# Optimization experiments

Measured on AMD Instinct MI355X. Metric: run time of the kernel, lower is better.

The kernel has to match this reference:

```python
import jax, jax.numpy as jnp
import numpy as np

B, S, HID = 2, 1024, 1024
NH, CH, HD = 16, 32, 64          # standard heads, constitutional heads, head_dim
TRUST = 64


def setup_inputs() -> dict:
    key = jax.random.key(0)
    ks = jax.random.split(key, 16)
    g = lambda k, sh, sc: jax.random.normal(k, sh, dtype=jnp.float32) * sc
    w = 1.0 / np.sqrt(HID)
    inp = {
        'hidden_states': g(ks[0], (B, S, HID), 1.0),
        'attention_mask': g(ks[1], (B, 1, S, S), 1.0),
        'trust_scores': jax.random.uniform(ks[2], (B, TRUST), dtype=jnp.float32),
        'Wq': g(ks[3], (HID, HID), w), 'bq': jnp.zeros((HID,), jnp.float32),
        'Wk': g(ks[4], (HID, HID), w), 'bk': jnp.zeros((HID,), jnp.float32),
        'Wv': g(ks[5], (HID, HID), w), 'bv': jnp.zeros((HID,), jnp.float32),
        'Wcq': g(ks[6], (HID, CH * HD), w), 'bcq': jnp.zeros((CH * HD,), jnp.float32),
        'Wck': g(ks[7], (HID, CH * HD), w), 'bck': jnp.zeros((CH * HD,), jnp.float32),
        'Wcv': g(ks[8], (HID, CH * HD), w), 'bcv': jnp.zeros((CH * HD,), jnp.float32),
        'Wt': g(ks[9], (TRUST, NH), 1.0 / np.sqrt(TRUST)), 'bt': jnp.zeros((NH,), jnp.float32),
        'Wo': g(ks[10], (HID, HID), w), 'bo': jnp.zeros((HID,), jnp.float32),
    }
    return inp


def reference(hidden_states, attention_mask, trust_scores,
              Wq, bq, Wk, bk, Wv, bv,
              Wcq, bcq, Wck, bck, Wcv, bcv,
              Wt, bt, Wo, bo):
    x = hidden_states
    scale = 1.0 / np.sqrt(HD).astype(np.float32)

    # standard QKV -> [B, NH, S, HD]
    q = (x @ Wq + bq).reshape(B, S, NH, HD)
    k = (x @ Wk + bk).reshape(B, S, NH, HD)
    v = (x @ Wv + bv).reshape(B, S, NH, HD)
    scores = jnp.einsum('bqhd,bkhd->bhqk', q, k) * scale  # [B,NH,S,S]
    scores = scores + attention_mask                       # additive mask

    # constitutional QKV -> [B, CH, S, HD]
    cq = (x @ Wcq + bcq).reshape(B, S, CH, HD)
    ck = (x @ Wck + bck).reshape(B, S, CH, HD)
    const_scores = jnp.einsum('bqhd,bkhd->bhqk', cq, ck) * scale  # [B,CH,S,S]

    # trust weighting: [B,TRUST] -> [B,NH] broadcast over [S,S]
    tw = trust_scores @ Wt + bt
    scores = scores * tw[:, :, None, None]

    # combine: per-head scores + mean over constitutional heads
    combined = scores + jnp.mean(const_scores, axis=1, keepdims=True)
    probs = jax.nn.softmax(combined, axis=-1)  # dropout is identity in eval

    context = jnp.einsum('bhqk,bkhd->bqhd', probs, v).reshape(B, S, HID)
    output = context @ Wo + bo
    return output, probs


if __name__ == '__main__':
    out, probs = reference(**setup_inputs())
    print(out.shape, probs.shape)
```

## Files before the change

kernel.cpp:

```cpp
#include <hip/hip_runtime.h>


typedef __bf16 bf16x8 __attribute__((ext_vector_type(8)));
typedef __bf16 bf16x4 __attribute__((ext_vector_type(4)));
typedef float  f32x4  __attribute__((ext_vector_type(4)));

static constexpr int Sq  = 1024;
static constexpr int LDP = 7168;

template<int ROWS>
__device__ __forceinline__ void stage_g(const __bf16* g, int ld, __bf16* s, int tid)
{
    constexpr int PER = (ROWS * 4) / 256;
    int w = tid >> 6, l = tid & 63;
#pragma unroll
    for (int i = 0; i < PER; i++) {
        int bc = w * 64 + i * 256;
        int chunk = bc + l;
        int row = chunk >> 2, part = (chunk & 3) * 8;
        const __bf16* gp = g + (size_t)row * ld + part;
        __bf16* sp = s + (size_t)bc * 8;
        __builtin_amdgcn_global_load_lds(
            (__attribute__((address_space(1))) void*)(gp),
            (__attribute__((address_space(3))) void*)(sp), 16, 0, 0);
    }
}

template<int BM, int BN, int EPI>
__global__ __launch_bounds__(256) void gemm_nt(
    const __bf16* __restrict__ A, int lda,
    const __bf16* __restrict__ B, int ldb,
    void* __restrict__ Cout, int ldc,
    const float* __restrict__ bias, int Ksz, float alpha)
{
    constexpr int WM = BM / 2, WN = BN / 2, FM = WM / 16, FN = WN / 16;
    __shared__ __bf16 As[BM][32];
    __shared__ __bf16 Bs[BN][32];
    int tid = threadIdx.x;
    int w = tid >> 6, l = tid & 63;
    int wr = w >> 1, wc = w & 1;
    int lr = l & 15, kp = (l >> 4) * 8;
    int bm = blockIdx.x * BM, bn = blockIdx.y * BN;
    int z = blockIdx.z;

    size_t zA = 0, zC = 0;
    if constexpr (EPI == 2) { zA = (size_t)z * 1024 * LDP; zC = (size_t)z * Sq * Sq; }

    f32x4 acc[FM][FN];
#pragma unroll
    for (int i = 0; i < FM; i++)
#pragma unroll
        for (int j = 0; j < FN; j++) acc[i][j] = (f32x4){0.f, 0.f, 0.f, 0.f};

    for (int k0 = 0; k0 < Ksz; k0 += 32) {
        stage_g<BM>(A + zA + (size_t)bm * lda + k0, lda, &As[0][0], tid);
        stage_g<BN>(B + zA + (size_t)bn * ldb + k0, ldb, &Bs[0][0], tid);
        __syncthreads();
        bf16x8 av[FM], bv[FN];
#pragma unroll
        for (int i = 0; i < FM; i++) av[i] = *(const bf16x8*)&As[wr * WM + i * 16 + lr][kp];
#pragma unroll
        for (int j = 0; j < FN; j++) bv[j] = *(const bf16x8*)&Bs[wc * WN + j * 16 + lr][kp];
#pragma unroll
        for (int i = 0; i < FM; i++)
#pragma unroll
            for (int j = 0; j < FN; j++)
                acc[i][j] = __builtin_amdgcn_mfma_f32_16x16x32_bf16(av[i], bv[j], acc[i][j], 0, 0, 0);
        __syncthreads();
    }

    int dr = (l >> 4) * 4, dc = l & 15;
#pragma unroll
    for (int i = 0; i < FM; i++)
#pragma unroll
        for (int j = 0; j < FN; j++)
#pragma unroll
            for (int t = 0; t < 4; t++) {
                int row = bm + wr * WM + i * 16 + dr + t;
                int col = bn + wc * WN + j * 16 + dc;
                float v = acc[i][j][t];
                size_t off = zC + (size_t)row * ldc + col;
                if constexpr (EPI == 0)      ((__bf16*)Cout)[off] = (__bf16)(v + bias[col]);
                else if constexpr (EPI == 1) ((float*)Cout)[off]  = v + bias[col];
                else                         ((float*)Cout)[off]  = v * alpha;
            }
}

__global__ __launch_bounds__(256, 2) void attn_fused(
    const __bf16* __restrict__ PROJ, const __bf16* __restrict__ Vt,
    const float* __restrict__ mask, const float* __restrict__ CM,
    const float* __restrict__ TW, float* __restrict__ probs,
    __bf16* __restrict__ CTXb)
{
    __shared__ float ctxred[4][64][36];
    __shared__ float red[32][4];

    int tid = threadIdx.x;
    int w = tid >> 6, l = tid & 63;
    int lr = l & 15, g = l >> 4, kp = g * 8;

    int bid = blockIdx.x;
    int low3 = bid & 7;
    int t6   = bid >> 3;
    int h    = t6 & 15;
    int g64  = (t6 >> 4) * 8 + low3;
    int b    = g64 >> 5;
    int bm   = (g64 & 31) * 32;
    int z    = b * 16 + h;

    const __bf16* Qg = PROJ + (size_t)(b * 1024 + bm) * LDP + h * 64;
    const __bf16* Kg = PROJ + (size_t)(b * 1024) * LDP + 1024 + h * 64;

    bf16x8 qv[2][2];
#pragma unroll
    for (int i = 0; i < 2; i++)
#pragma unroll
        for (int kk = 0; kk < 2; kk++)
            qv[i][kk] = *(const bf16x8*)(Qg + (size_t)(i * 16 + lr) * LDP + kk * 32 + kp);

    f32x4 acc[2][16];
#pragma unroll
    for (int i = 0; i < 2; i++)
#pragma unroll
        for (int j = 0; j < 16; j++) acc[i][j] = (f32x4){0.f, 0.f, 0.f, 0.f};

#pragma unroll
    for (int j = 0; j < 16; j++) {
        const __bf16* Kt = Kg + (size_t)(w * 256 + j * 16 + lr) * LDP;
        bf16x8 k0 = *(const bf16x8*)(Kt + kp);
        bf16x8 k1 = *(const bf16x8*)(Kt + 32 + kp);
#pragma unroll
        for (int i = 0; i < 2; i++) {
            acc[i][j] = __builtin_amdgcn_mfma_f32_16x16x32_bf16(k0, qv[i][0], acc[i][j], 0, 0, 0);
            acc[i][j] = __builtin_amdgcn_mfma_f32_16x16x32_bf16(k1, qv[i][1], acc[i][j], 0, 0, 0);
        }
    }

    float twv = TW[z];
    float s1 = 0.125f * twv;
    const float* Mb  = mask + (size_t)b * Sq * Sq;
    const float* CMb = CM   + (size_t)b * Sq * Sq;

    float mx[2];
#pragma unroll
    for (int i = 0; i < 2; i++) {
        size_t rb = (size_t)(bm + i * 16 + lr) * 1024;
        float mm = -1e30f;
#pragma unroll
        for (int j = 0; j < 16; j++) {
            int off = w * 256 + j * 16 + g * 4;
            f32x4 mk = *(const f32x4*)(Mb + rb + off);
            f32x4 c4 = *(const f32x4*)(CMb + rb + off);
#pragma unroll
            for (int t = 0; t < 4; t++) {
                float lv = fmaf(acc[i][j][t], s1, fmaf(mk[t], twv, c4[t]));
                acc[i][j][t] = lv;
                mm = fmaxf(mm, lv);
            }
        }
        mm = fmaxf(mm, __shfl_xor(mm, 16));
        mm = fmaxf(mm, __shfl_xor(mm, 32));
        mx[i] = mm;
    }
    if (g == 0) { red[lr][w] = mx[0]; red[16 + lr][w] = mx[1]; }
    __syncthreads();
#pragma unroll
    for (int i = 0; i < 2; i++) {
        const float* r = red[i * 16 + lr];
        mx[i] = fmaxf(fmaxf(r[0], r[1]), fmaxf(r[2], r[3]));
    }

    float sm[2];
#pragma unroll
    for (int i = 0; i < 2; i++) {
        float s = 0.f;
#pragma unroll
        for (int j = 0; j < 16; j++)
#pragma unroll
            for (int t = 0; t < 4; t++) {
                float e = __expf(acc[i][j][t] - mx[i]);
                acc[i][j][t] = e;
                s += e;
            }
        s += __shfl_xor(s, 16);
        s += __shfl_xor(s, 32);
        sm[i] = s;
    }
    __syncthreads();
    if (g == 0) { red[lr][w] = sm[0]; red[16 + lr][w] = sm[1]; }
    __syncthreads();

    float inv[2];
#pragma unroll
    for (int i = 0; i < 2; i++) {
        const float* r = red[i * 16 + lr];
        inv[i] = 1.0f / (r[0] + r[1] + r[2] + r[3]);
    }

    const __bf16* Vg = Vt + ((size_t)b * 1024 + h * 64) * 1024;
    float* Pg = probs + (size_t)z * Sq * Sq;
    f32x4 c[2][4];
#pragma unroll
    for (int i = 0; i < 2; i++)
#pragma unroll
        for (int nt = 0; nt < 4; nt++) c[i][nt] = (f32x4){0.f, 0.f, 0.f, 0.f};

#pragma unroll
    for (int j = 0; j < 16; j++) {
        int kb = w * 256 + j * 16 + g * 4;
        bf16x4 vb[4];
#pragma unroll
        for (int nt = 0; nt < 4; nt++)
            vb[nt] = *(const bf16x4*)(Vg + (size_t)(nt * 16 + lr) * 1024 + kb);
#pragma unroll
        for (int i = 0; i < 2; i++) {
            f32x4 p;
#pragma unroll
            for (int t = 0; t < 4; t++) p[t] = acc[i][j][t] * inv[i];
            *(f32x4*)(Pg + (size_t)(bm + i * 16 + lr) * 1024 + kb) = p;
            bf16x4 pa;
#pragma unroll
            for (int t = 0; t < 4; t++) pa[t] = (__bf16)p[t];
#pragma unroll
            for (int nt = 0; nt < 4; nt++)
                asm volatile("v_mfma_f32_16x16x16_bf16 %0, %1, %2, %0"
                             : "+v"(c[i][nt]) : "v"(pa), "v"(vb[nt]));
        }
    }

#pragma unroll
    for (int i = 0; i < 2; i++)
#pragma unroll
        for (int nt = 0; nt < 4; nt++)
            *(f32x4*)&ctxred[w][nt * 16 + lr][i * 16 + g * 4] = c[i][nt];
    __syncthreads();

    int q8 = tid & 31, dq = (tid >> 5) * 8;
    bf16x8 o;
#pragma unroll
    for (int e = 0; e < 8; e++) {
        int d = dq + e;
        float s = ctxred[0][d][q8] + ctxred[1][d][q8] + ctxred[2][d][q8] + ctxred[3][d][q8];
        o[e] = (__bf16)s;
    }
    *(bf16x8*)&CTXb[(size_t)(b * 1024 + bm + q8) * 1024 + h * 64 + dq] = o;
}

__global__ __launch_bounds__(256) void convert_f32_bf16(
    const float* __restrict__ src, __bf16* __restrict__ dst)
{
    int i = blockIdx.x * 256 + threadIdx.x;
    size_t base = (size_t)i * 8;
    float4 a = *(const float4*)(src + base);
    float4 b = *(const float4*)(src + base + 4);
    bf16x8 o;
    o[0] = (__bf16)a.x; o[1] = (__bf16)a.y; o[2] = (__bf16)a.z; o[3] = (__bf16)a.w;
    o[4] = (__bf16)b.x; o[5] = (__bf16)b.y; o[6] = (__bf16)b.z; o[7] = (__bf16)b.w;
    *(bf16x8*)(dst + base) = o;
}

__global__ __launch_bounds__(256) void transpose_all(
    const float* __restrict__ Wq, const float* __restrict__ Wk,
    const float* __restrict__ Wv, const float* __restrict__ Wcq,
    const float* __restrict__ Wck, const float* __restrict__ Wo,
    __bf16* __restrict__ Wall, __bf16* __restrict__ WoT)
{
    int zz = blockIdx.z;
    const float* src;
    int nof, ld;
    switch (zz) {
        case 0: src = Wq;  nof = 0;    ld = 1024; break;
        case 1: src = Wk;  nof = 0;    ld = 1024; break;
        case 2: src = Wv;  nof = 0;    ld = 1024; break;
        case 3: src = Wcq; nof = 0;    ld = 2048; break;
        case 4: src = Wcq; nof = 1024; ld = 2048; break;
        case 5: src = Wck; nof = 0;    ld = 2048; break;
        case 6: src = Wck; nof = 1024; ld = 2048; break;
        default: src = Wo; nof = 0;    ld = 1024; break;
    }
    __bf16* dst = (zz == 7) ? WoT : Wall + (size_t)zz * 1024 * 1024;

    __shared__ float t[32][33];
    int tx = threadIdx.x, ty = threadIdx.y;
    int n0 = blockIdx.x * 32, k0 = blockIdx.y * 32;
#pragma unroll
    for (int i = 0; i < 4; i++)
        t[ty + i * 8][tx] = src[(size_t)(k0 + ty + i * 8) * ld + nof + n0 + tx];
    __syncthreads();
#pragma unroll
    for (int i = 0; i < 4; i++)
        dst[(size_t)(n0 + ty + i * 8) * 1024 + k0 + tx] = (__bf16)t[tx][ty + i * 8];
}

__global__ __launch_bounds__(256) void transpose_v(
    const __bf16* __restrict__ PROJ, __bf16* __restrict__ Vt)
{
    int b = blockIdx.z;
    __shared__ __bf16 t[32][33];
    int tx = threadIdx.x, ty = threadIdx.y;
    int s0 = blockIdx.x * 32, d0 = blockIdx.y * 32;
#pragma unroll
    for (int i = 0; i < 4; i++)
        t[ty + i * 8][tx] = PROJ[(size_t)(b * 1024 + s0 + ty + i * 8) * LDP + 2048 + d0 + tx];
    __syncthreads();
#pragma unroll
    for (int i = 0; i < 4; i++)
        Vt[(size_t)(b * 1024 + d0 + ty + i * 8) * 1024 + s0 + tx] = t[tx][ty + i * 8];
}

__global__ void pack_bias(const float* bq, const float* bk, const float* bv,
                          const float* bcq, const float* bck, float* ball)
{
    int i = blockIdx.x * 256 + threadIdx.x;
    if (i >= LDP) return;
    float v;
    if (i < 1024) v = bq[i];
    else if (i < 2048) v = bk[i - 1024];
    else if (i < 3072) v = bv[i - 2048];
    else if (i < 5120) v = bcq[i - 3072];
    else v = bck[i - 5120];
    ball[i] = v;
}

__global__ void tw_kernel(const float* __restrict__ trust, const float* __restrict__ Wt,
                          const float* __restrict__ bt, float* __restrict__ tw)
{
    int i = threadIdx.x;
    if (i >= 32) return;
    int b = i >> 4, h = i & 15;
    float s = bt[h];
    for (int k = 0; k < 64; k++) s += trust[b * 64 + k] * Wt[k * 16 + h];
    tw[i] = s;
}

extern "C" void kernel_launch(void* const* d_in, const int* in_sizes, int n_in,
                              void* d_out, int out_size, void* d_ws, size_t ws_size,
                              hipStream_t stream)
{
    (void)in_sizes; (void)n_in; (void)out_size; (void)ws_size;
    const float* x     = (const float*)d_in[0];
    const float* mask  = (const float*)d_in[1];
    const float* trust = (const float*)d_in[2];
    const float* Wq  = (const float*)d_in[3];  const float* bq  = (const float*)d_in[4];
    const float* Wk  = (const float*)d_in[5];  const float* bk  = (const float*)d_in[6];
    const float* Wv  = (const float*)d_in[7];  const float* bv  = (const float*)d_in[8];
    const float* Wcq = (const float*)d_in[9];  const float* bcq = (const float*)d_in[10];
    const float* Wck = (const float*)d_in[11]; const float* bck = (const float*)d_in[12];
    const float* Wt  = (const float*)d_in[15]; const float* bt  = (const float*)d_in[16];
    const float* Wo  = (const float*)d_in[17]; const float* bo  = (const float*)d_in[18];

    float* out   = (float*)d_out;
    float* probs = out + (size_t)2 * Sq * 1024;

    constexpr size_t MB = 1u << 20;
    char* w8 = (char*)d_ws;
    __bf16* xb   = (__bf16*)(w8 + 0 * MB);
    __bf16* Wall = (__bf16*)(w8 + 4 * MB);
    float*  ball = (float*) (w8 + 19 * MB);
    float*  TW   = (float*) (w8 + 19 * MB + 65536);
    __bf16* WoT  = (__bf16*)(w8 + 19 * MB + 131072);
    __bf16* PROJ = (__bf16*)(w8 + 22 * MB);
    __bf16* Vt   = (__bf16*)(w8 + 50 * MB);
    float*  CM   = (float*) (w8 + 54 * MB);
    __bf16* CTXb = (__bf16*)(w8 + 0 * MB);

    dim3 tb(32, 8);

    convert_f32_bf16<<<1024, 256, 0, stream>>>(x, xb);
    transpose_all<<<dim3(32, 32, 8), tb, 0, stream>>>(Wq, Wk, Wv, Wcq, Wck, Wo, Wall, WoT);
    pack_bias<<<28, 256, 0, stream>>>(bq, bk, bv, bcq, bck, ball);
    tw_kernel<<<1, 64, 0, stream>>>(trust, Wt, bt, TW);

    gemm_nt<128, 128, 0><<<dim3(16, 56, 1), 256, 0, stream>>>(
        xb, 1024, Wall, 1024, PROJ, LDP, ball, 1024, 0.f);

    transpose_v<<<dim3(32, 32, 2), tb, 0, stream>>>(PROJ, Vt);

    gemm_nt<128, 64, 2><<<dim3(8, 16, 2), 256, 0, stream>>>(
        PROJ + 3072, LDP, PROJ + 5120, LDP, CM, 1024, nullptr, 2048, 0.00390625f);

    attn_fused<<<dim3(1024), 256, 0, stream>>>(PROJ, Vt, mask, CM, TW, probs, CTXb);

    gemm_nt<64, 64, 1><<<dim3(32, 16, 1), 256, 0, stream>>>(
        CTXb, 1024, WoT, 1024, out, 1024, bo, 1024, 0.f);
}
```

Before: 216.5 us.

## Pre-pack K and V into MFMA fragment order for coalesced attention loads

Replaces the V transpose kernel with two packing kernels that rewrite K and V per head into the exact per-lane MFMA fragment order. The attention kernel can then read K and V with contiguous, fully coalesced vector loads instead of strided rows of the wide projection buffer. It also swaps the inline-asm 16x16x16 MFMA for the compiler builtin when available, which lets the compiler schedule it. The cost is an extra launch and extra workspace traffic to write the packed copies, and pack_v uses scalar strided gathers.

Measured after the change: 204.9 us. -5.4%, faster.

```diff
diff --git a/kernel.cpp b/kernel.cpp
--- a/kernel.cpp
+++ b/kernel.cpp
@@ -3,10 +3,29 @@
 
 typedef __bf16 bf16x8 __attribute__((ext_vector_type(8)));
 typedef __bf16 bf16x4 __attribute__((ext_vector_type(4)));
+typedef short  s16x4  __attribute__((ext_vector_type(4)));
 typedef float  f32x4  __attribute__((ext_vector_type(4)));
 
 static constexpr int Sq  = 1024;
 static constexpr int LDP = 7168;
+
+#if defined(__has_builtin)
+#  if __has_builtin(__builtin_amdgcn_mfma_f32_16x16x16bf16_1k)
+#    define HAVE_MFMA16B 1
+#  endif
+#endif
+
+__device__ __forceinline__ void mfma16(f32x4& c, bf16x4 a, bf16x4 b)
+{
+#ifdef HAVE_MFMA16B
+    union { bf16x4 h; s16x4 s; } ua, ub;
+    ua.h = a; ub.h = b;
+    c = __builtin_amdgcn_mfma_f32_16x16x16bf16_1k(ua.s, ub.s, c, 0, 0, 0);
+#else
+    asm volatile("v_mfma_f32_16x16x16_bf16 %0, %1, %2, %0"
+                 : "+v"(c) : "v"(a), "v"(b));
+#endif
+}
 
 template<int ROWS>
 __device__ __forceinline__ void stage_g(const __bf16* g, int ld, __bf16* s, int tid)
@@ -87,7 +106,8 @@
 }
 
 __global__ __launch_bounds__(256, 2) void attn_fused(
-    const __bf16* __restrict__ PROJ, const __bf16* __restrict__ Vt,
+    const __bf16* __restrict__ PROJ, const __bf16* __restrict__ Kp,
+    const __bf16* __restrict__ Vp,
     const float* __restrict__ mask, const float* __restrict__ CM,
     const float* __restrict__ TW, float* __restrict__ probs,
     __bf16* __restrict__ CTXb)
@@ -108,8 +128,9 @@
     int bm   = (g64 & 31) * 32;
     int z    = b * 16 + h;
 
-    const __bf16* Qg = PROJ + (size_t)(b * 1024 + bm) * LDP + h * 64;
-    const __bf16* Kg = PROJ + (size_t)(b * 1024) * LDP + 1024 + h * 64;
+    const __bf16* Qg  = PROJ + (size_t)(b * 1024 + bm) * LDP + h * 64;
+    const __bf16* Kzp = Kp + (size_t)z * 65536;
+    const __bf16* Vzp = Vp + (size_t)z * 65536;
 
     bf16x8 qv[2][2];
 #pragma unroll
@@ -126,9 +147,9 @@
 
 #pragma unroll
     for (int j = 0; j < 16; j++) {
-        const __bf16* Kt = Kg + (size_t)(w * 256 + j * 16 + lr) * LDP;
-        bf16x8 k0 = *(const bf16x8*)(Kt + kp);
-        bf16x8 k1 = *(const bf16x8*)(Kt + 32 + kp);
+        int T = w * 16 + j;
+        bf16x8 k0 = *(const bf16x8*)(Kzp + ((size_t)(T * 2 + 0) * 64 + l) * 8);
+        bf16x8 k1 = *(const bf16x8*)(Kzp + ((size_t)(T * 2 + 1) * 64 + l) * 8);
 #pragma unroll
         for (int i = 0; i < 2; i++) {
             acc[i][j] = __builtin_amdgcn_mfma_f32_16x16x32_bf16(k0, qv[i][0], acc[i][j], 0, 0, 0);
@@ -197,7 +218,6 @@
         inv[i] = 1.0f / (r[0] + r[1] + r[2] + r[3]);
     }
 
-    const __bf16* Vg = Vt + ((size_t)b * 1024 + h * 64) * 1024;
     float* Pg = probs + (size_t)z * Sq * Sq;
     f32x4 c[2][4];
 #pragma unroll
@@ -207,11 +227,12 @@
 
 #pragma unroll
     for (int j = 0; j < 16; j++) {
+        int T = w * 16 + j;
         int kb = w * 256 + j * 16 + g * 4;
         bf16x4 vb[4];
 #pragma unroll
         for (int nt = 0; nt < 4; nt++)
-            vb[nt] = *(const bf16x4*)(Vg + (size_t)(nt * 16 + lr) * 1024 + kb);
+            vb[nt] = *(const bf16x4*)(Vzp + ((size_t)(T * 4 + nt) * 64 + l) * 4);
 #pragma unroll
         for (int i = 0; i < 2; i++) {
             f32x4 p;
@@ -223,8 +244,7 @@
             for (int t = 0; t < 4; t++) pa[t] = (__bf16)p[t];
 #pragma unroll
             for (int nt = 0; nt < 4; nt++)
-                asm volatile("v_mfma_f32_16x16x16_bf16 %0, %1, %2, %0"
-                             : "+v"(c[i][nt]) : "v"(pa), "v"(vb[nt]));
+                mfma16(c[i][nt], pa, vb[nt]);
         }
     }
 
@@ -292,20 +312,31 @@
         dst[(size_t)(n0 + ty + i * 8) * 1024 + k0 + tx] = (__bf16)t[tx][ty + i * 8];
 }
 
-__global__ __launch_bounds__(256) void transpose_v(
-    const __bf16* __restrict__ PROJ, __bf16* __restrict__ Vt)
-{
-    int b = blockIdx.z;
-    __shared__ __bf16 t[32][33];
-    int tx = threadIdx.x, ty = threadIdx.y;
-    int s0 = blockIdx.x * 32, d0 = blockIdx.y * 32;
-#pragma unroll
-    for (int i = 0; i < 4; i++)
-        t[ty + i * 8][tx] = PROJ[(size_t)(b * 1024 + s0 + ty + i * 8) * LDP + 2048 + d0 + tx];
-    __syncthreads();
-#pragma unroll
-    for (int i = 0; i < 4; i++)
-        Vt[(size_t)(b * 1024 + d0 + ty + i * 8) * 1024 + s0 + tx] = t[tx][ty + i * 8];
+__global__ __launch_bounds__(256) void pack_k(
+    const __bf16* __restrict__ PROJ, __bf16* __restrict__ Kp)
+{
+    int z = blockIdx.y, b = z >> 4, h = z & 15;
+    int t = threadIdx.x;
+    int T  = blockIdx.x * 2 + (t >> 7);
+    int kk = (t >> 6) & 1, g = (t >> 4) & 3, lr = t & 15;
+    bf16x8 v = *(const bf16x8*)(PROJ + (size_t)(b * 1024 + T * 16 + lr) * LDP
+                                + 1024 + h * 64 + kk * 32 + g * 8);
+    *(bf16x8*)(Kp + (size_t)z * 65536 + ((size_t)(T * 2 + kk) * 64 + g * 16 + lr) * 8) = v;
+}
+
+__global__ __launch_bounds__(256) void pack_v(
+    const __bf16* __restrict__ PROJ, __bf16* __restrict__ Vp)
+{
+    int z = blockIdx.y, b = z >> 4, h = z & 15;
+    int T = blockIdx.x;
+    int t = threadIdx.x;
+    int nt = t >> 6, g = (t >> 4) & 3, lr = t & 15;
+    bf16x4 v;
+#pragma unroll
+    for (int e = 0; e < 4; e++)
+        v[e] = PROJ[(size_t)(b * 1024 + T * 16 + g * 4 + e) * LDP
+                    + 2048 + h * 64 + nt * 16 + lr];
+    *(bf16x4*)(Vp + (size_t)z * 65536 + ((size_t)(T * 4 + nt) * 64 + g * 16 + lr) * 4) = v;
 }
 
 __global__ void pack_bias(const float* bq, const float* bk, const float* bv,
@@ -360,8 +391,9 @@
     float*  TW   = (float*) (w8 + 19 * MB + 65536);
     __bf16* WoT  = (__bf16*)(w8 + 19 * MB + 131072);
     __bf16* PROJ = (__bf16*)(w8 + 22 * MB);
-    __bf16* Vt   = (__bf16*)(w8 + 50 * MB);
+    __bf16* Vp   = (__bf16*)(w8 + 50 * MB);
     float*  CM   = (float*) (w8 + 54 * MB);
+    __bf16* Kp   = (__bf16*)(w8 + 62 * MB);
     __bf16* CTXb = (__bf16*)(w8 + 0 * MB);
 
     dim3 tb(32, 8);
@@ -374,12 +406,13 @@
     gemm_nt<128, 128, 0><<<dim3(16, 56, 1), 256, 0, stream>>>(
         xb, 1024, Wall, 1024, PROJ, LDP, ball, 1024, 0.f);
 
-    transpose_v<<<dim3(32, 32, 2), tb, 0, stream>>>(PROJ, Vt);
+    pack_k<<<dim3(32, 32), 256, 0, stream>>>(PROJ, Kp);
+    pack_v<<<dim3(64, 32), 256, 0, stream>>>(PROJ, Vp);
 
     gemm_nt<128, 64, 2><<<dim3(8, 16, 2), 256, 0, stream>>>(
         PROJ + 3072, LDP, PROJ + 5120, LDP, CM, 1024, nullptr, 2048, 0.00390625f);
 
-    attn_fused<<<dim3(1024), 256, 0, stream>>>(PROJ, Vt, mask, CM, TW, probs, CTXb);
+    attn_fused<<<dim3(1024), 256, 0, stream>>>(PROJ, Kp, Vp, mask, CM, TW, probs, CTXb);
 
     gemm_nt<64, 64, 1><<<dim3(32, 16, 1), 256, 0, stream>>>(
         CTXb, 1024, WoT, 1024, out, 1024, bo, 1024, 0.f);
```
